# Performance work log

Hardware: AMD Instinct MI355X
Metric: run time of the kernel (lower is better)

## Reference

```python
import jax, jax.numpy as jnp
import numpy as np

WIN_SIZE = 7
K1 = 0.01
K2 = 0.03
COV_NORM = WIN_SIZE / (WIN_SIZE - 1)
N = 16777216


def _box(v):
    # valid-mode box filter, kernel = ones(WIN_SIZE)/WIN_SIZE (symmetric, so flip is a no-op)
    w = jnp.ones((WIN_SIZE,), dtype=v.dtype) / WIN_SIZE
    return jnp.convolve(v, w, mode='valid')


def setup_inputs() -> dict:
    key = jax.random.key(0)
    kx, ky = jax.random.split(key)
    x = jax.random.normal(kx, (N,), dtype=jnp.float32)
    y = jax.random.normal(ky, (N,), dtype=jnp.float32)
    return {"x": x, "y": y}


def reference(x, y):
    data_range = jnp.max(y)
    C1 = (K1 * data_range) ** 2
    C2 = (K2 * data_range) ** 2
    ux = _box(x)
    uy = _box(y)
    uxx = _box(x * x)
    uyy = _box(y * y)
    uxy = _box(x * y)
    vx = COV_NORM * (uxx - ux * ux)
    vy = COV_NORM * (uyy - uy * uy)
    vxy = COV_NORM * (uxy - ux * uy)
    A1 = 2 * ux * uy + C1
    A2 = 2 * vxy + C2
    B1 = ux ** 2 + uy ** 2 + C1
    B2 = vx + vy + C2
    S = A1 * A2 / (B1 * B2)
    return jnp.mean(S)
```

## Files before the change

kernel.cpp:

```cpp
#include <hip/hip_runtime.h>
#include <math.h>

#define WIN 7
#define WPT 8
#define BLK 256
#define NB 2048
#define GSTRIDE (NB * BLK)

__device__ __forceinline__ float max4(float4 v) {
    return fmaxf(fmaxf(v.x, v.y), fmaxf(v.z, v.w));
}

__device__ __forceinline__ float ssim_win(float P, float Q, float sxx, float syy, float sxy,
                                          float c1, float c1d, float c2a, float c2b) {
    float t1 = P * Q;
    float u  = fmaf(P, P, Q * Q);
    float A1 = fmaf(t1, 4.0f, c1d);
    float A2 = fmaf(sxy, 7.0f, c2a - t1);
    float B1 = u + c1;
    float B2 = fmaf(sxx + syy, 7.0f, c2b - u);
    return (A1 * A2) * __builtin_amdgcn_rcpf(B1 * B2);
}

__device__ __forceinline__ float compute_item(float4 x0, float4 x1, float4 x2, float4 x3,
                                              float4 y0, float4 y1, float4 y2, float4 y3,
                                              float c1, float c1d, float c2a, float c2b) {
    float xv[16] = {x0.x,x0.y,x0.z,x0.w, x1.x,x1.y,x1.z,x1.w,
                    x2.x,x2.y,x2.z,x2.w, x3.x,x3.y,x3.z,x3.w};
    float yv[16] = {y0.x,y0.y,y0.z,y0.w, y1.x,y1.y,y1.z,y1.w,
                    y2.x,y2.y,y2.z,y2.w, y3.x,y3.y,y3.z,y3.w};
    float P = 0.f, Q = 0.f, sxx = 0.f, syy = 0.f, sxy = 0.f;
    #pragma unroll
    for (int k = 0; k < WIN; k++) {
        float a = xv[k], b = yv[k];
        P += a; Q += b;
        sxx = fmaf(a, a, sxx);
        syy = fmaf(b, b, syy);
        sxy = fmaf(a, b, sxy);
    }
    float r = 0.f;
    #pragma unroll
    for (int j = 0; j < WPT; j++) {
        r += ssim_win(P, Q, sxx, syy, sxy, c1, c1d, c2a, c2b);
        if (j < WPT - 1) {
            float ao = xv[j], an = xv[j + WIN];
            float bo = yv[j], bn = yv[j + WIN];
            P += an - ao;
            Q += bn - bo;
            sxx += fmaf(an, an, -(ao * ao));
            syy += fmaf(bn, bn, -(bo * bo));
            sxy += fmaf(an, bn, -(ao * bo));
        }
    }
    return r;
}

__global__ __launch_bounds__(BLK) void kmax_partial(const float* __restrict__ y, int n,
                                                    float* __restrict__ outMax) {
    const int gid = blockIdx.x * BLK + threadIdx.x;
    const int n4 = n >> 2;
    const float4* y4 = (const float4*)y;
    float m0 = -__builtin_huge_valf(), m1 = m0;
    int i = gid;
    for (; i + GSTRIDE < n4; i += 2 * GSTRIDE) {
        float4 a = y4[i];
        float4 b = y4[i + GSTRIDE];
        m0 = fmaxf(m0, max4(a));
        m1 = fmaxf(m1, max4(b));
    }
    for (; i < n4; i += GSTRIDE) m0 = fmaxf(m0, max4(y4[i]));
    for (int j = (n4 << 2) + gid; j < n; j += GSTRIDE) m0 = fmaxf(m0, y[j]);
    float m = fmaxf(m0, m1);
    #pragma unroll
    for (int off = 32; off; off >>= 1) m = fmaxf(m, __shfl_xor(m, off));
    __shared__ float sm[4];
    if ((threadIdx.x & 63) == 0) sm[threadIdx.x >> 6] = m;
    __syncthreads();
    if (threadIdx.x == 0)
        outMax[blockIdx.x] = fmaxf(fmaxf(sm[0], sm[1]), fmaxf(sm[2], sm[3]));
}

__global__ __launch_bounds__(BLK) void kssim(const float* __restrict__ x,
                                             const float* __restrict__ y,
                                             const float* __restrict__ partMax, int n,
                                             int ninterior, int nfull, int rem,
                                             float* __restrict__ blockSums) {
    const int tid = threadIdx.x;
    const int gid = blockIdx.x * BLK + tid;
    __shared__ float sm[4];

    float mm = -__builtin_huge_valf();
    #pragma unroll
    for (int i = 0; i < NB / BLK; i++) mm = fmaxf(mm, partMax[i * BLK + tid]);
    #pragma unroll
    for (int off = 32; off; off >>= 1) mm = fmaxf(mm, __shfl_xor(mm, off));
    if ((tid & 63) == 0) sm[tid >> 6] = mm;
    __syncthreads();
    const float dr = fmaxf(fmaxf(sm[0], sm[1]), fmaxf(sm[2], sm[3]));
    const float C1 = (0.01f * dr) * (0.01f * dr);
    const float C2 = (0.03f * dr) * (0.03f * dr);
    const float c1  = 49.0f * C1;
    const float c1d = 2.0f * c1;
    const float c2a = 21.0f * C2;
    const float c2b = 42.0f * C2;

    float acc = 0.0f;
    int g = gid;
    float4 ax0, ax1, ax2, ax3, ay0, ay1, ay2, ay3;
    if (g < ninterior) {
        const float4* px = (const float4*)(x + g * WPT);
        ax0 = px[0]; ax1 = px[1]; ax2 = px[2]; ax3 = px[3];
        const float4* py = (const float4*)(y + g * WPT);
        ay0 = py[0]; ay1 = py[1]; ay2 = py[2]; ay3 = py[3];
    }
    for (int k = 0; k < nfull; k++) {
        const int gn = g + GSTRIDE;
        const bool nextExists = (k + 1 < nfull) || (gid < rem);
        float4 bx0, bx1, bx2, bx3, by0, by1, by2, by3;
        if (nextExists) {
            const float4* px = (const float4*)(x + gn * WPT);
            bx0 = px[0]; bx1 = px[1]; bx2 = px[2]; bx3 = px[3];
            const float4* py = (const float4*)(y + gn * WPT);
            by0 = py[0]; by1 = py[1]; by2 = py[2]; by3 = py[3];
        }
        acc += compute_item(ax0, ax1, ax2, ax3, ay0, ay1, ay2, ay3, c1, c1d, c2a, c2b);
        ax0 = bx0; ax1 = bx1; ax2 = bx2; ax3 = bx3;
        ay0 = by0; ay1 = by1; ay2 = by2; ay3 = by3;
        g = gn;
    }
    if (gid < rem)
        acc += compute_item(ax0, ax1, ax2, ax3, ay0, ay1, ay2, ay3, c1, c1d, c2a, c2b);

    if (gid == 0) {
        const int nw = n - (WIN - 1);
        for (int w = ninterior * WPT; w < nw; ++w) {
            float P = 0.f, Q = 0.f, sxx = 0.f, syy = 0.f, sxy = 0.f;
            for (int k = 0; k < WIN; k++) {
                float a = x[w + k], b = y[w + k];
                P += a; Q += b;
                sxx = fmaf(a, a, sxx);
                syy = fmaf(b, b, syy);
                sxy = fmaf(a, b, sxy);
            }
            acc += ssim_win(P, Q, sxx, syy, sxy, c1, c1d, c2a, c2b);
        }
    }

    #pragma unroll
    for (int off = 32; off; off >>= 1) acc += __shfl_xor(acc, off);
    __syncthreads();
    if ((tid & 63) == 0) sm[tid >> 6] = acc;
    __syncthreads();
    if (tid == 0)
        blockSums[blockIdx.x] = (sm[0] + sm[1]) + (sm[2] + sm[3]);
}

__global__ __launch_bounds__(BLK) void kfinal(const float* __restrict__ blockSums, int nb,
                                              float* __restrict__ out, int nw) {
    double s = 0.0;
    for (int i = threadIdx.x; i < nb; i += BLK) s += (double)blockSums[i];
    #pragma unroll
    for (int off = 32; off; off >>= 1) s += __shfl_xor(s, off);
    __shared__ double sd[4];
    if ((threadIdx.x & 63) == 0) sd[threadIdx.x >> 6] = s;
    __syncthreads();
    if (threadIdx.x == 0)
        out[0] = (float)(((sd[0] + sd[1]) + (sd[2] + sd[3])) / (double)nw);
}

extern "C" void kernel_launch(void* const* d_in, const int* in_sizes, int n_in,
                              void* d_out, int out_size, void* d_ws, size_t ws_size,
                              hipStream_t stream) {
    const float* x = (const float*)d_in[0];
    const float* y = (const float*)d_in[1];
    float* out = (float*)d_out;
    int n = in_sizes[0];
    int nw = n - (WIN - 1);
    int ninterior = (n >= 16) ? ((n - 16) / WPT + 1) : 0;
    int nfull = ninterior / GSTRIDE;
    int rem   = ninterior - nfull * GSTRIDE;

    float* wsf = (float*)d_ws;
    float* partMax   = wsf;
    float* blockSums = wsf + NB;

    kmax_partial<<<NB, BLK, 0, stream>>>(y, n, partMax);
    kssim<<<NB, BLK, 0, stream>>>(x, y, partMax, n, ninterior, nfull, rem, blockSums);
    kfinal<<<1, BLK, 0, stream>>>(blockSums, NB, out, nw);
}
```

Measured before the change: 43.58 us.

## Stage tiles through double-buffered LDS and fuse final reduction via atomics

The SSIM kernel now loads contiguous tiles of x and y (1024 elements plus an 8-element halo) into double-buffered shared memory with coalesced float4 loads. Each thread computes 4 windows from LDS, where before each thread read 16 overlapping elements per 8 windows directly from global memory. The separate final reduction kernel is removed: block sums are converted to fixed-point and atomically added, with a last-block counter writing the mean. This saves a launch and reduces redundant global reads, at the cost of an extra LDS round trip, a barrier per tile, and fixed-point rounding in the sum.

```diff
diff --git a/kernel.cpp b/kernel.cpp
--- a/kernel.cpp
+++ b/kernel.cpp
@@ -2,10 +2,12 @@
 #include <math.h>
 
 #define WIN 7
-#define WPT 8
+#define W 4
 #define BLK 256
+#define TILE (BLK * W)
 #define NB 2048
-#define GSTRIDE (NB * BLK)
+#define NF4 ((TILE + 8) / 4)
+#define FIX_SCALE 274877906944.0
 
 __device__ __forceinline__ float max4(float4 v) {
     return fmaxf(fmaxf(v.x, v.y), fmaxf(v.z, v.w));
@@ -22,54 +24,36 @@
     return (A1 * A2) * __builtin_amdgcn_rcpf(B1 * B2);
 }
 
-__device__ __forceinline__ float compute_item(float4 x0, float4 x1, float4 x2, float4 x3,
-                                              float4 y0, float4 y1, float4 y2, float4 y3,
-                                              float c1, float c1d, float c2a, float c2b) {
-    float xv[16] = {x0.x,x0.y,x0.z,x0.w, x1.x,x1.y,x1.z,x1.w,
-                    x2.x,x2.y,x2.z,x2.w, x3.x,x3.y,x3.z,x3.w};
-    float yv[16] = {y0.x,y0.y,y0.z,y0.w, y1.x,y1.y,y1.z,y1.w,
-                    y2.x,y2.y,y2.z,y2.w, y3.x,y3.y,y3.z,y3.w};
-    float P = 0.f, Q = 0.f, sxx = 0.f, syy = 0.f, sxy = 0.f;
-    #pragma unroll
-    for (int k = 0; k < WIN; k++) {
-        float a = xv[k], b = yv[k];
-        P += a; Q += b;
-        sxx = fmaf(a, a, sxx);
-        syy = fmaf(b, b, syy);
-        sxy = fmaf(a, b, sxy);
-    }
-    float r = 0.f;
-    #pragma unroll
-    for (int j = 0; j < WPT; j++) {
-        r += ssim_win(P, Q, sxx, syy, sxy, c1, c1d, c2a, c2b);
-        if (j < WPT - 1) {
-            float ao = xv[j], an = xv[j + WIN];
-            float bo = yv[j], bn = yv[j + WIN];
-            P += an - ao;
-            Q += bn - bo;
-            sxx += fmaf(an, an, -(ao * ao));
-            syy += fmaf(bn, bn, -(bo * bo));
-            sxy += fmaf(an, bn, -(ao * bo));
-        }
-    }
-    return r;
+__device__ __forceinline__ float4 gload(const float* __restrict__ p, int f4, int n) {
+    int f = f4 * 4;
+    if (f + 4 <= n) return *(const float4*)(p + f);
+    float4 v = {0.f, 0.f, 0.f, 0.f};
+    if (f + 0 < n) v.x = p[f + 0];
+    if (f + 1 < n) v.y = p[f + 1];
+    if (f + 2 < n) v.z = p[f + 2];
+    if (f + 3 < n) v.w = p[f + 3];
+    return v;
 }
 
 __global__ __launch_bounds__(BLK) void kmax_partial(const float* __restrict__ y, int n,
-                                                    float* __restrict__ outMax) {
+                                                    float* __restrict__ outMax,
+                                                    unsigned long long* __restrict__ accum,
+                                                    unsigned int* __restrict__ counter) {
+    if (blockIdx.x == 0 && threadIdx.x == 0) { *accum = 0ull; *counter = 0u; }
     const int gid = blockIdx.x * BLK + threadIdx.x;
     const int n4 = n >> 2;
+    const int GS = NB * BLK;
     const float4* y4 = (const float4*)y;
     float m0 = -__builtin_huge_valf(), m1 = m0;
     int i = gid;
-    for (; i + GSTRIDE < n4; i += 2 * GSTRIDE) {
+    for (; i + GS < n4; i += 2 * GS) {
         float4 a = y4[i];
-        float4 b = y4[i + GSTRIDE];
+        float4 b = y4[i + GS];
         m0 = fmaxf(m0, max4(a));
         m1 = fmaxf(m1, max4(b));
     }
-    for (; i < n4; i += GSTRIDE) m0 = fmaxf(m0, max4(y4[i]));
-    for (int j = (n4 << 2) + gid; j < n; j += GSTRIDE) m0 = fmaxf(m0, y[j]);
+    for (; i < n4; i += GS) m0 = fmaxf(m0, max4(y4[i]));
+    for (int j = (n4 << 2) + gid; j < n; j += GS) m0 = fmaxf(m0, y[j]);
     float m = fmaxf(m0, m1);
     #pragma unroll
     for (int off = 32; off; off >>= 1) m = fmaxf(m, __shfl_xor(m, off));
@@ -83,11 +67,13 @@
 __global__ __launch_bounds__(BLK) void kssim(const float* __restrict__ x,
                                              const float* __restrict__ y,
                                              const float* __restrict__ partMax, int n,
-                                             int ninterior, int nfull, int rem,
-                                             float* __restrict__ blockSums) {
+                                             int ntiles, int nw,
+                                             unsigned long long* __restrict__ accum,
+                                             unsigned int* __restrict__ counter,
+                                             float* __restrict__ out) {
     const int tid = threadIdx.x;
-    const int gid = blockIdx.x * BLK + tid;
     __shared__ float sm[4];
+    __shared__ float4 lb[2][2][NF4];
 
     float mm = -__builtin_huge_valf();
     #pragma unroll
@@ -105,44 +91,89 @@
     const float c2b = 42.0f * C2;
 
     float acc = 0.0f;
-    int g = gid;
-    float4 ax0, ax1, ax2, ax3, ay0, ay1, ay2, ay3;
-    if (g < ninterior) {
-        const float4* px = (const float4*)(x + g * WPT);
-        ax0 = px[0]; ax1 = px[1]; ax2 = px[2]; ax3 = px[3];
-        const float4* py = (const float4*)(y + g * WPT);
-        ay0 = py[0]; ay1 = py[1]; ay2 = py[2]; ay3 = py[3];
-    }
-    for (int k = 0; k < nfull; k++) {
-        const int gn = g + GSTRIDE;
-        const bool nextExists = (k + 1 < nfull) || (gid < rem);
-        float4 bx0, bx1, bx2, bx3, by0, by1, by2, by3;
-        if (nextExists) {
-            const float4* px = (const float4*)(x + gn * WPT);
-            bx0 = px[0]; bx1 = px[1]; bx2 = px[2]; bx3 = px[3];
-            const float4* py = (const float4*)(y + gn * WPT);
-            by0 = py[0]; by1 = py[1]; by2 = py[2]; by3 = py[3];
-        }
-        acc += compute_item(ax0, ax1, ax2, ax3, ay0, ay1, ay2, ay3, c1, c1d, c2a, c2b);
-        ax0 = bx0; ax1 = bx1; ax2 = bx2; ax3 = bx3;
-        ay0 = by0; ay1 = by1; ay2 = by2; ay3 = by3;
-        g = gn;
-    }
-    if (gid < rem)
-        acc += compute_item(ax0, ax1, ax2, ax3, ay0, ay1, ay2, ay3, c1, c1d, c2a, c2b);
-
-    if (gid == 0) {
-        const int nw = n - (WIN - 1);
-        for (int w = ninterior * WPT; w < nw; ++w) {
-            float P = 0.f, Q = 0.f, sxx = 0.f, syy = 0.f, sxy = 0.f;
-            for (int k = 0; k < WIN; k++) {
-                float a = x[w + k], b = y[w + k];
-                P += a; Q += b;
-                sxx = fmaf(a, a, sxx);
-                syy = fmaf(b, b, syy);
-                sxy = fmaf(a, b, sxy);
+    int tile = blockIdx.x;
+    float4 ax0, ax1, ay0, ay1;
+    if (tile < ntiles) {
+        int b4 = tile * (TILE / 4);
+        ax0 = gload(x, b4 + tid, n);
+        ay0 = gload(y, b4 + tid, n);
+        if (tid < NF4 - BLK) {
+            ax1 = gload(x, b4 + BLK + tid, n);
+            ay1 = gload(y, b4 + BLK + tid, n);
+        }
+    }
+    int it = 0;
+    for (; tile < ntiles; tile += NB, ++it) {
+        const int buf = it & 1;
+        lb[buf][0][tid] = ax0;
+        lb[buf][1][tid] = ay0;
+        if (tid < NF4 - BLK) {
+            lb[buf][0][BLK + tid] = ax1;
+            lb[buf][1][BLK + tid] = ay1;
+        }
+        const int ntile = tile + NB;
+        if (ntile < ntiles) {
+            int b4 = ntile * (TILE / 4);
+            ax0 = gload(x, b4 + tid, n);
+            ay0 = gload(y, b4 + tid, n);
+            if (tid < NF4 - BLK) {
+                ax1 = gload(x, b4 + BLK + tid, n);
+                ay1 = gload(y, b4 + BLK + tid, n);
             }
-            acc += ssim_win(P, Q, sxx, syy, sxy, c1, c1d, c2a, c2b);
+        }
+        __syncthreads();
+
+        const float* lx = (const float*)&lb[buf][0][0];
+        const float* ly = (const float*)&lb[buf][1][0];
+        float4 f0 = *(const float4*)(lx + 4 * tid);
+        float4 f1 = *(const float4*)(lx + 4 * tid + 4);
+        float4 f2 = *(const float4*)(lx + 4 * tid + 8);
+        float4 g0 = *(const float4*)(ly + 4 * tid);
+        float4 g1 = *(const float4*)(ly + 4 * tid + 4);
+        float4 g2 = *(const float4*)(ly + 4 * tid + 8);
+        float xv[12] = {f0.x,f0.y,f0.z,f0.w, f1.x,f1.y,f1.z,f1.w, f2.x,f2.y,f2.z,f2.w};
+        float yv[12] = {g0.x,g0.y,g0.z,g0.w, g1.x,g1.y,g1.z,g1.w, g2.x,g2.y,g2.z,g2.w};
+
+        float P = 0.f, Q = 0.f, sxx = 0.f, syy = 0.f, sxy = 0.f;
+        #pragma unroll
+        for (int k = 0; k < WIN; k++) {
+            float a = xv[k], b = yv[k];
+            P += a; Q += b;
+            sxx = fmaf(a, a, sxx);
+            syy = fmaf(b, b, syy);
+            sxy = fmaf(a, b, sxy);
+        }
+        const int T = tile * TILE;
+        if (T + TILE + 8 <= n) {
+            #pragma unroll
+            for (int j = 0; j < W; j++) {
+                acc += ssim_win(P, Q, sxx, syy, sxy, c1, c1d, c2a, c2b);
+                if (j < W - 1) {
+                    float ao = xv[j], an = xv[j + WIN];
+                    float bo = yv[j], bn = yv[j + WIN];
+                    P += an - ao;
+                    Q += bn - bo;
+                    sxx += fmaf(an, an, -(ao * ao));
+                    syy += fmaf(bn, bn, -(bo * bo));
+                    sxy += fmaf(an, bn, -(ao * bo));
+                }
+            }
+        } else {
+            const int w0 = T + 4 * tid;
+            #pragma unroll
+            for (int j = 0; j < W; j++) {
+                if (w0 + j < nw)
+                    acc += ssim_win(P, Q, sxx, syy, sxy, c1, c1d, c2a, c2b);
+                if (j < W - 1) {
+                    float ao = xv[j], an = xv[j + WIN];
+                    float bo = yv[j], bn = yv[j + WIN];
+                    P += an - ao;
+                    Q += bn - bo;
+                    sxx += fmaf(an, an, -(ao * ao));
+                    syy += fmaf(bn, bn, -(bo * bo));
+                    sxy += fmaf(an, bn, -(ao * bo));
+                }
+            }
         }
     }
 
@@ -151,21 +182,18 @@
     __syncthreads();
     if ((tid & 63) == 0) sm[tid >> 6] = acc;
     __syncthreads();
-    if (tid == 0)
-        blockSums[blockIdx.x] = (sm[0] + sm[1]) + (sm[2] + sm[3]);
-}
-
-__global__ __launch_bounds__(BLK) void kfinal(const float* __restrict__ blockSums, int nb,
-                                              float* __restrict__ out, int nw) {
-    double s = 0.0;
-    for (int i = threadIdx.x; i < nb; i += BLK) s += (double)blockSums[i];
-    #pragma unroll
-    for (int off = 32; off; off >>= 1) s += __shfl_xor(s, off);
-    __shared__ double sd[4];
-    if ((threadIdx.x & 63) == 0) sd[threadIdx.x >> 6] = s;
-    __syncthreads();
-    if (threadIdx.x == 0)
-        out[0] = (float)(((sd[0] + sd[1]) + (sd[2] + sd[3])) / (double)nw);
+    if (tid == 0) {
+        float bs = (sm[0] + sm[1]) + (sm[2] + sm[3]);
+        long long q = (long long)rint((double)bs * FIX_SCALE);
+        atomicAdd(accum, (unsigned long long)q);
+        __threadfence();
+        unsigned int prev = atomicAdd(counter, 1u);
+        if (prev == (unsigned int)(gridDim.x - 1)) {
+            unsigned long long tot = atomicAdd(accum, 0ull);
+            double s = (double)(long long)tot / FIX_SCALE;
+            out[0] = (float)(s / (double)nw);
+        }
+    }
 }
 
 extern "C" void kernel_launch(void* const* d_in, const int* in_sizes, int n_in,
@@ -176,15 +204,12 @@
     float* out = (float*)d_out;
     int n = in_sizes[0];
     int nw = n - (WIN - 1);
-    int ninterior = (n >= 16) ? ((n - 16) / WPT + 1) : 0;
-    int nfull = ninterior / GSTRIDE;
-    int rem   = ninterior - nfull * GSTRIDE;
-
-    float* wsf = (float*)d_ws;
-    float* partMax   = wsf;
-    float* blockSums = wsf + NB;
-
-    kmax_partial<<<NB, BLK, 0, stream>>>(y, n, partMax);
-    kssim<<<NB, BLK, 0, stream>>>(x, y, partMax, n, ninterior, nfull, rem, blockSums);
-    kfinal<<<1, BLK, 0, stream>>>(blockSums, NB, out, nw);
-}
+    int ntiles = (nw + TILE - 1) / TILE;
+
+    unsigned long long* accum = (unsigned long long*)d_ws;
+    unsigned int* counter = (unsigned int*)((char*)d_ws + 8);
+    float* partMax = (float*)((char*)d_ws + 256);
+
+    kmax_partial<<<NB, BLK, 0, stream>>>(y, n, partMax, accum, counter);
+    kssim<<<NB, BLK, 0, stream>>>(x, y, partMax, n, ntiles, nw, accum, counter, out);
+}
```

Measured after the change: 95.13 us. +118.3%, slower.

## Stage SSIM tiles in padded LDS with one block per tile

Applied to the files above, without the earlier changes.

Replaces the grid-stride loop, in which each thread loaded 16 overlapping floats per 8 windows directly from global memory, with one block per 2048-element tile. Each block cooperatively loads the tile plus its halo into bank-conflict-padded shared memory, then each thread reads its 16 values from LDS. This removes the 2x redundant global reads and the serial tail handled by a single thread. The cost is a much larger grid (8192 blocks), so every block re-reads the 2048 partial maxima, and the software prefetch pipelining is lost.

```diff
diff --git a/kernel.cpp b/kernel.cpp
--- a/kernel.cpp
+++ b/kernel.cpp
@@ -4,8 +4,12 @@
 #define WIN 7
 #define WPT 8
 #define BLK 256
+#define TILEW (BLK * WPT)
+#define TFLOATS (TILEW + 16)
 #define NB 2048
-#define GSTRIDE (NB * BLK)
+#define LWORDS (TFLOATS + 4 * ((TFLOATS + 31) / 32))
+
+__device__ __forceinline__ int lidx(int f) { return f + ((f >> 5) << 2); }
 
 __device__ __forceinline__ float max4(float4 v) {
     return fmaxf(fmaxf(v.x, v.y), fmaxf(v.z, v.w));
@@ -22,54 +26,36 @@
     return (A1 * A2) * __builtin_amdgcn_rcpf(B1 * B2);
 }
 
-__device__ __forceinline__ float compute_item(float4 x0, float4 x1, float4 x2, float4 x3,
-                                              float4 y0, float4 y1, float4 y2, float4 y3,
-                                              float c1, float c1d, float c2a, float c2b) {
-    float xv[16] = {x0.x,x0.y,x0.z,x0.w, x1.x,x1.y,x1.z,x1.w,
-                    x2.x,x2.y,x2.z,x2.w, x3.x,x3.y,x3.z,x3.w};
-    float yv[16] = {y0.x,y0.y,y0.z,y0.w, y1.x,y1.y,y1.z,y1.w,
-                    y2.x,y2.y,y2.z,y2.w, y3.x,y3.y,y3.z,y3.w};
-    float P = 0.f, Q = 0.f, sxx = 0.f, syy = 0.f, sxy = 0.f;
-    #pragma unroll
-    for (int k = 0; k < WIN; k++) {
-        float a = xv[k], b = yv[k];
-        P += a; Q += b;
-        sxx = fmaf(a, a, sxx);
-        syy = fmaf(b, b, syy);
-        sxy = fmaf(a, b, sxy);
-    }
-    float r = 0.f;
-    #pragma unroll
-    for (int j = 0; j < WPT; j++) {
-        r += ssim_win(P, Q, sxx, syy, sxy, c1, c1d, c2a, c2b);
-        if (j < WPT - 1) {
-            float ao = xv[j], an = xv[j + WIN];
-            float bo = yv[j], bn = yv[j + WIN];
-            P += an - ao;
-            Q += bn - bo;
-            sxx += fmaf(an, an, -(ao * ao));
-            syy += fmaf(bn, bn, -(bo * bo));
-            sxy += fmaf(an, bn, -(ao * bo));
-        }
-    }
-    return r;
+__device__ __forceinline__ float4 gload(const float* __restrict__ p, int f4, int n) {
+    int f = f4 * 4;
+    if (f + 4 <= n) return *(const float4*)(p + f);
+    float4 v = {0.f, 0.f, 0.f, 0.f};
+    if (f + 0 < n) v.x = p[f + 0];
+    if (f + 1 < n) v.y = p[f + 1];
+    if (f + 2 < n) v.z = p[f + 2];
+    return v;
+}
+
+__device__ __forceinline__ void store4(float* lds, int f, float4 v) {
+    *(float4*)&lds[lidx(f)] = v;
 }
 
 __global__ __launch_bounds__(BLK) void kmax_partial(const float* __restrict__ y, int n,
                                                     float* __restrict__ outMax) {
     const int gid = blockIdx.x * BLK + threadIdx.x;
     const int n4 = n >> 2;
+    const int GS = NB * BLK;
     const float4* y4 = (const float4*)y;
     float m0 = -__builtin_huge_valf(), m1 = m0;
     int i = gid;
-    for (; i + GSTRIDE < n4; i += 2 * GSTRIDE) {
+    for (; i + GS < n4; i += 2 * GS) {
         float4 a = y4[i];
-        float4 b = y4[i + GSTRIDE];
+        float4 b = y4[i + GS];
         m0 = fmaxf(m0, max4(a));
         m1 = fmaxf(m1, max4(b));
     }
-    for (; i < n4; i += GSTRIDE) m0 = fmaxf(m0, max4(y4[i]));
-    for (int j = (n4 << 2) + gid; j < n; j += GSTRIDE) m0 = fmaxf(m0, y[j]);
+    for (; i < n4; i += GS) m0 = fmaxf(m0, max4(y4[i]));
+    for (int j = (n4 << 2) + gid; j < n; j += GS) m0 = fmaxf(m0, y[j]);
     float m = fmaxf(m0, m1);
     #pragma unroll
     for (int off = 32; off; off >>= 1) m = fmaxf(m, __shfl_xor(m, off));
@@ -83,10 +69,11 @@
 __global__ __launch_bounds__(BLK) void kssim(const float* __restrict__ x,
                                              const float* __restrict__ y,
                                              const float* __restrict__ partMax, int n,
-                                             int ninterior, int nfull, int rem,
+                                             int nw,
                                              float* __restrict__ blockSums) {
     const int tid = threadIdx.x;
-    const int gid = blockIdx.x * BLK + tid;
+    const int T = blockIdx.x * TILEW;
+    __shared__ float lx[LWORDS], ly[LWORDS];
     __shared__ float sm[4];
 
     float mm = -__builtin_huge_valf();
@@ -104,45 +91,86 @@
     const float c2a = 21.0f * C2;
     const float c2b = 42.0f * C2;
 
+    const bool full = (T + TFLOATS <= n);
+    if (full) {
+        const float4* px = (const float4*)(x + T);
+        const float4* py = (const float4*)(y + T);
+        float4 a0 = px[tid], a1 = px[tid + 256];
+        float4 b0 = py[tid], b1 = py[tid + 256];
+        float4 a2, b2;
+        if (tid < TFLOATS / 4 - 512) { a2 = px[512 + tid]; b2 = py[512 + tid]; }
+        store4(lx, 4 * tid, a0);
+        store4(lx, 4 * (tid + 256), a1);
+        store4(ly, 4 * tid, b0);
+        store4(ly, 4 * (tid + 256), b1);
+        if (tid < TFLOATS / 4 - 512) {
+            store4(lx, 4 * (512 + tid), a2);
+            store4(ly, 4 * (512 + tid), b2);
+        }
+    } else {
+        const int t4 = T >> 2;
+        for (int i = tid; i < TFLOATS / 4; i += BLK) {
+            store4(lx, 4 * i, gload(x, t4 + i, n));
+            store4(ly, 4 * i, gload(y, t4 + i, n));
+        }
+    }
+    __syncthreads();
+
     float acc = 0.0f;
-    int g = gid;
-    float4 ax0, ax1, ax2, ax3, ay0, ay1, ay2, ay3;
-    if (g < ninterior) {
-        const float4* px = (const float4*)(x + g * WPT);
-        ax0 = px[0]; ax1 = px[1]; ax2 = px[2]; ax3 = px[3];
-        const float4* py = (const float4*)(y + g * WPT);
-        ay0 = py[0]; ay1 = py[1]; ay2 = py[2]; ay3 = py[3];
-    }
-    for (int k = 0; k < nfull; k++) {
-        const int gn = g + GSTRIDE;
-        const bool nextExists = (k + 1 < nfull) || (gid < rem);
-        float4 bx0, bx1, bx2, bx3, by0, by1, by2, by3;
-        if (nextExists) {
-            const float4* px = (const float4*)(x + gn * WPT);
-            bx0 = px[0]; bx1 = px[1]; bx2 = px[2]; bx3 = px[3];
-            const float4* py = (const float4*)(y + gn * WPT);
-            by0 = py[0]; by1 = py[1]; by2 = py[2]; by3 = py[3];
-        }
-        acc += compute_item(ax0, ax1, ax2, ax3, ay0, ay1, ay2, ay3, c1, c1d, c2a, c2b);
-        ax0 = bx0; ax1 = bx1; ax2 = bx2; ax3 = bx3;
-        ay0 = by0; ay1 = by1; ay2 = by2; ay3 = by3;
-        g = gn;
-    }
-    if (gid < rem)
-        acc += compute_item(ax0, ax1, ax2, ax3, ay0, ay1, ay2, ay3, c1, c1d, c2a, c2b);
-
-    if (gid == 0) {
-        const int nw = n - (WIN - 1);
-        for (int w = ninterior * WPT; w < nw; ++w) {
-            float P = 0.f, Q = 0.f, sxx = 0.f, syy = 0.f, sxy = 0.f;
-            for (int k = 0; k < WIN; k++) {
-                float a = x[w + k], b = y[w + k];
-                P += a; Q += b;
-                sxx = fmaf(a, a, sxx);
-                syy = fmaf(b, b, syy);
-                sxy = fmaf(a, b, sxy);
+    {
+        const int f0 = 8 * tid;
+        float4 v0 = *(const float4*)&lx[lidx(f0)];
+        float4 v1 = *(const float4*)&lx[lidx(f0 + 4)];
+        float4 v2 = *(const float4*)&lx[lidx(f0 + 8)];
+        float4 v3 = *(const float4*)&lx[lidx(f0 + 12)];
+        float4 w0 = *(const float4*)&ly[lidx(f0)];
+        float4 w1 = *(const float4*)&ly[lidx(f0 + 4)];
+        float4 w2 = *(const float4*)&ly[lidx(f0 + 8)];
+        float4 w3 = *(const float4*)&ly[lidx(f0 + 12)];
+        float xv[16] = {v0.x,v0.y,v0.z,v0.w, v1.x,v1.y,v1.z,v1.w,
+                        v2.x,v2.y,v2.z,v2.w, v3.x,v3.y,v3.z,v3.w};
+        float yv[16] = {w0.x,w0.y,w0.z,w0.w, w1.x,w1.y,w1.z,w1.w,
+                        w2.x,w2.y,w2.z,w2.w, w3.x,w3.y,w3.z,w3.w};
+
+        float P = 0.f, Q = 0.f, sxx = 0.f, syy = 0.f, sxy = 0.f;
+        #pragma unroll
+        for (int k = 0; k < WIN; k++) {
+            float a = xv[k], b = yv[k];
+            P += a; Q += b;
+            sxx = fmaf(a, a, sxx);
+            syy = fmaf(b, b, syy);
+            sxy = fmaf(a, b, sxy);
+        }
+        if (T + TILEW + (WIN - 1) <= n) {
+            #pragma unroll
+            for (int j = 0; j < WPT; j++) {
+                acc += ssim_win(P, Q, sxx, syy, sxy, c1, c1d, c2a, c2b);
+                if (j < WPT - 1) {
+                    float ao = xv[j], an = xv[j + WIN];
+                    float bo = yv[j], bn = yv[j + WIN];
+                    P += an - ao;
+                    Q += bn - bo;
+                    sxx += fmaf(an, an, -(ao * ao));
+                    syy += fmaf(bn, bn, -(bo * bo));
+                    sxy += fmaf(an, bn, -(ao * bo));
+                }
             }
-            acc += ssim_win(P, Q, sxx, syy, sxy, c1, c1d, c2a, c2b);
+        } else {
+            const int wbase = T + 8 * tid;
+            #pragma unroll
+            for (int j = 0; j < WPT; j++) {
+                if (wbase + j < nw)
+                    acc += ssim_win(P, Q, sxx, syy, sxy, c1, c1d, c2a, c2b);
+                if (j < WPT - 1) {
+                    float ao = xv[j], an = xv[j + WIN];
+                    float bo = yv[j], bn = yv[j + WIN];
+                    P += an - ao;
+                    Q += bn - bo;
+                    sxx += fmaf(an, an, -(ao * ao));
+                    syy += fmaf(bn, bn, -(bo * bo));
+                    sxy += fmaf(an, bn, -(ao * bo));
+                }
+            }
         }
     }
 
@@ -176,15 +204,13 @@
     float* out = (float*)d_out;
     int n = in_sizes[0];
     int nw = n - (WIN - 1);
-    int ninterior = (n >= 16) ? ((n - 16) / WPT + 1) : 0;
-    int nfull = ninterior / GSTRIDE;
-    int rem   = ninterior - nfull * GSTRIDE;
+    int ntiles = (nw + TILEW - 1) / TILEW;
 
     float* wsf = (float*)d_ws;
     float* partMax   = wsf;
     float* blockSums = wsf + NB;
 
     kmax_partial<<<NB, BLK, 0, stream>>>(y, n, partMax);
-    kssim<<<NB, BLK, 0, stream>>>(x, y, partMax, n, ninterior, nfull, rem, blockSums);
-    kfinal<<<1, BLK, 0, stream>>>(blockSums, NB, out, nw);
-}
+    kssim<<<ntiles, BLK, 0, stream>>>(x, y, partMax, n, nw, blockSums);
+    kfinal<<<1, BLK, 0, stream>>>(blockSums, ntiles, out, nw);
+}
```

After: 49.41 us. +13.4%, slower.
